# Performance work log

Hardware: AMD Instinct MI355X
Metric: run time of the kernel (lower is better)

The kernel has to match this reference:

```python
import jax, jax.numpy as jnp
import numpy as np

B, S, H = 32, 2048, 512

def setup_inputs() -> dict:
    key = jax.random.key(0)
    k1, k2, k3, k4 = jax.random.split(key, 4)
    Y = jax.random.normal(k1, (B, S, H), dtype=jnp.float32)
    mask_Y = jnp.ones((B, S), dtype=jnp.float32)
    W = jax.random.normal(k2, (H, H), dtype=jnp.float32)
    b = jax.random.normal(k3, (H,), dtype=jnp.float32)
    w = jax.random.normal(k4, (H,), dtype=jnp.float32)
    return {"Y": Y, "mask_Y": mask_Y, "W": W, "b": b, "w": w}

def reference(Y, mask_Y, W, b, w):
    # u: [B,S,H] = tanh(Y @ W + b)
    u = jnp.tanh(jnp.einsum('bsh,hd->bsd', Y, W) + b)
    # scores: [B,S] = u . w, masked with large negative additive bias
    scores = jnp.einsum('bsh,h->bs', u, w) - 1000.0 * (1.0 - mask_Y)
    alpha = jax.nn.softmax(scores, axis=1)  # [B,S]
    # c_star: [B,H] = attention-weighted sum of Y
    c_star = jnp.einsum('bs,bsh->bh', alpha, Y)
    return c_star
```

## Files before the change

### kernel.cpp

```cpp
#include <hip/hip_runtime.h>
#include <hip/hip_bf16.h>


#define Bsz 32
#define Ssz 2048
#define Hsz 512
#define Msz (Bsz * Ssz)

using half8   = __attribute__((ext_vector_type(8))) _Float16;
using floatx4 = __attribute__((ext_vector_type(4))) float;

__device__ __forceinline__ void llds16(void* l, const void* g) {
  __builtin_amdgcn_global_load_lds((const __attribute__((address_space(1))) void*)g,
                                   (__attribute__((address_space(3))) void*)l, 16, 0, 0);
}

__device__ __forceinline__ float fast_tanh(float x) {
  const float e = __expf(2.f * x);
  return 1.f - 2.f / (e + 1.f);
}

__global__ __launch_bounds__(256) void wsplit_k(const float* __restrict__ W,
                                                _Float16* __restrict__ Wt) {
  __shared__ float tile[32][33];
  const int bx = blockIdx.x & 15, by = blockIdx.x >> 4;
  const int tx = threadIdx.x & 31, ty = threadIdx.x >> 5;
#pragma unroll
  for (int i = 0; i < 4; ++i)
    tile[ty + 8 * i][tx] = W[(size_t)(by * 32 + ty + 8 * i) * Hsz + bx * 32 + tx];
  __syncthreads();
#pragma unroll
  for (int i = 0; i < 4; ++i) {
    const int n = bx * 32 + ty + 8 * i;
    const int k = by * 32 + tx;
    Wt[(size_t)n * Hsz + k] = (_Float16)tile[tx][ty + 8 * i];
  }
}

__global__ __launch_bounds__(256) void gemm_score_k(const float* __restrict__ Y,
                                                    const _Float16* __restrict__ Wt,
                                                    const float* __restrict__ bvec,
                                                    const float* __restrict__ wvec,
                                                    float* __restrict__ scores4) {
  __shared__ __align__(16) float    As[128 * 32];
  __shared__ __align__(16) _Float16 Bs[128 * 32];
  const int tid = threadIdx.x;
  const int lane = tid & 63, wv = tid >> 6;
  const int wr = wv >> 1, wc = wv & 1;
  const int lr = lane & 15, lq = lane >> 4;
  const int g = blockIdx.x;
  const int x = g & 7, q = g >> 3;
  const int nblk = q & 3;
  const int mblk = (q >> 2) * 8 + x;

  floatx4 acc[4][4];
#pragma unroll
  for (int rf = 0; rf < 4; ++rf)
#pragma unroll
    for (int cf = 0; cf < 4; ++cf)
      acc[rf][cf] = (floatx4){0.f, 0.f, 0.f, 0.f};

  const float* aY = Y + (size_t)mblk * 128 * Hsz;
  const _Float16* bW = Wt + (size_t)nblk * 128 * Hsz;

  for (int it = 0; it < 16; ++it) {
    const int k0 = it * 32;
#pragma unroll
    for (int i = 0; i < 4; ++i) {
      const int cb = i * 256 + wv * 64;
      const int p = cb + lane;
      const int row = p >> 3;
      const int gc = (p & 7) ^ (row & 7);
      llds16(&As[cb * 4], aY + (size_t)row * Hsz + k0 + gc * 4);
    }
#pragma unroll
    for (int i = 0; i < 2; ++i) {
      const int cb = i * 256 + wv * 64;
      const int p = cb + lane;
      const int row = p >> 2;
      const int gc = (p & 3) ^ ((row >> 1) & 3);
      llds16(&Bs[cb * 8], bW + (size_t)row * Hsz + k0 + gc * 8);
    }
    __syncthreads();

    half8 a[4], bf[4];
#pragma unroll
    for (int rf = 0; rf < 4; ++rf) {
      const int ar = wr * 64 + rf * 16 + lr;
      const int s0 = (lq * 2) ^ (ar & 7);
      const float4 flo = *(const float4*)&As[ar * 32 + s0 * 4];
      const float4 fhi = *(const float4*)&As[ar * 32 + (s0 ^ 1) * 4];
      half8 h;
      h[0] = (_Float16)flo.x; h[1] = (_Float16)flo.y;
      h[2] = (_Float16)flo.z; h[3] = (_Float16)flo.w;
      h[4] = (_Float16)fhi.x; h[5] = (_Float16)fhi.y;
      h[6] = (_Float16)fhi.z; h[7] = (_Float16)fhi.w;
      a[rf] = h;
    }
#pragma unroll
    for (int cf = 0; cf < 4; ++cf) {
      const int nr = wc * 64 + cf * 16 + lr;
      bf[cf] = *(const half8*)&Bs[nr * 32 + (lq ^ ((nr >> 1) & 3)) * 8];
    }
#pragma unroll
    for (int rf = 0; rf < 4; ++rf)
#pragma unroll
      for (int cf = 0; cf < 4; ++cf)
        acc[rf][cf] = __builtin_amdgcn_mfma_f32_16x16x32_f16(a[rf], bf[cf], acc[rf][cf], 0, 0, 0);
    __syncthreads();
  }

  float bb[4], ww[4];
  const int colbase = nblk * 128 + wc * 64;
#pragma unroll
  for (int cf = 0; cf < 4; ++cf) {
    const int col = colbase + cf * 16 + lr;
    bb[cf] = bvec[col];
    ww[cf] = wvec[col];
  }
  float* red = (float*)As;
#pragma unroll
  for (int rf = 0; rf < 4; ++rf) {
#pragma unroll
    for (int r = 0; r < 4; ++r) {
      float v = 0.f;
#pragma unroll
      for (int cf = 0; cf < 4; ++cf)
        v += fast_tanh(acc[rf][cf][r] + bb[cf]) * ww[cf];
      v += __shfl_xor(v, 1, 16);
      v += __shfl_xor(v, 2, 16);
      v += __shfl_xor(v, 4, 16);
      v += __shfl_xor(v, 8, 16);
      if (lr == 0)
        red[(wr * 64 + rf * 16 + lq * 4 + r) * 2 + wc] = v;
    }
  }
  __syncthreads();
  if (tid < 128)
    scores4[(size_t)nblk * Msz + mblk * 128 + tid] = red[2 * tid] + red[2 * tid + 1];
}

__global__ __launch_bounds__(256) void softmax_k(const float* __restrict__ scores4,
                                                 const float* __restrict__ mask,
                                                 float* __restrict__ alpha) {
  const int b = blockIdx.x, t = threadIdx.x;
  const int lane = t & 63, wv = t >> 6;
  float s[8];
  float mx = -3.4e38f;
#pragma unroll
  for (int i = 0; i < 8; ++i) {
    const int idx = b * Ssz + i * 256 + t;
    float v = scores4[idx] + scores4[Msz + idx] + scores4[2 * Msz + idx] + scores4[3 * Msz + idx];
    v -= 1000.f * (1.f - mask[idx]);
    s[i] = v;
    mx = fmaxf(mx, v);
  }
  for (int off = 32; off > 0; off >>= 1) mx = fmaxf(mx, __shfl_xor(mx, off, 64));
  __shared__ float rm[4], rs[4];
  if (lane == 0) rm[wv] = mx;
  __syncthreads();
  mx = fmaxf(fmaxf(rm[0], rm[1]), fmaxf(rm[2], rm[3]));
  float sum = 0.f;
#pragma unroll
  for (int i = 0; i < 8; ++i) {
    s[i] = __expf(s[i] - mx);
    sum += s[i];
  }
  for (int off = 32; off > 0; off >>= 1) sum += __shfl_xor(sum, off, 64);
  if (lane == 0) rs[wv] = sum;
  __syncthreads();
  sum = rs[0] + rs[1] + rs[2] + rs[3];
  const float inv = 1.f / sum;
#pragma unroll
  for (int i = 0; i < 8; ++i) alpha[b * Ssz + i * 256 + t] = s[i] * inv;
}

__global__ __launch_bounds__(256) void wsum1_k(const float* __restrict__ alpha,
                                               const float* __restrict__ Y,
                                               float* __restrict__ partial) {
  const int b = blockIdx.x >> 5, sc = blockIdx.x & 31;
  const int t = threadIdx.x, lane = t & 63, wv = t >> 6;
  __shared__ float part[4 * 512];
  const int s0 = sc * 64 + wv * 16;
  const float* al = alpha + b * Ssz + s0;
  const float4* Yb = (const float4*)(Y + ((size_t)b * Ssz + s0) * Hsz);
  float a0 = 0.f, a1 = 0.f, a2 = 0.f, a3 = 0.f, a4 = 0.f, a5 = 0.f, a6 = 0.f, a7 = 0.f;
#pragma unroll 4
  for (int r = 0; r < 16; ++r) {
    const float a = al[r];
    const float4 y0 = Yb[r * 128 + lane * 2];
    const float4 y1 = Yb[r * 128 + lane * 2 + 1];
    a0 = fmaf(a, y0.x, a0); a1 = fmaf(a, y0.y, a1);
    a2 = fmaf(a, y0.z, a2); a3 = fmaf(a, y0.w, a3);
    a4 = fmaf(a, y1.x, a4); a5 = fmaf(a, y1.y, a5);
    a6 = fmaf(a, y1.z, a6); a7 = fmaf(a, y1.w, a7);
  }
  part[wv * 512 + 0 * 64 + lane] = a0;
  part[wv * 512 + 1 * 64 + lane] = a1;
  part[wv * 512 + 2 * 64 + lane] = a2;
  part[wv * 512 + 3 * 64 + lane] = a3;
  part[wv * 512 + 4 * 64 + lane] = a4;
  part[wv * 512 + 5 * 64 + lane] = a5;
  part[wv * 512 + 6 * 64 + lane] = a6;
  part[wv * 512 + 7 * 64 + lane] = a7;
  __syncthreads();
#pragma unroll
  for (int i = 0; i < 2; ++i) {
    const int h = i * 256 + t;
    const int idx = (h & 7) * 64 + (h >> 3);
    partial[((size_t)(b * 32 + sc)) * Hsz + h] =
        part[idx] + part[512 + idx] + part[1024 + idx] + part[1536 + idx];
  }
}

__global__ __launch_bounds__(256) void wsum2_k(const float* __restrict__ partial,
                                               float* __restrict__ out) {
  const int b = blockIdx.x >> 1;
  const int h = (blockIdx.x & 1) * 256 + threadIdx.x;
  float s = 0.f;
#pragma unroll 8
  for (int sc = 0; sc < 32; ++sc)
    s += partial[((size_t)(b * 32 + sc)) * Hsz + h];
  out[b * Hsz + h] = s;
}

extern "C" void kernel_launch(void* const* d_in, const int* in_sizes, int n_in,
                              void* d_out, int out_size, void* d_ws, size_t ws_size,
                              hipStream_t stream) {
  (void)in_sizes; (void)n_in; (void)out_size; (void)ws_size;
  const float* Y    = (const float*)d_in[0];
  const float* mask = (const float*)d_in[1];
  const float* W    = (const float*)d_in[2];
  const float* bvec = (const float*)d_in[3];
  const float* wvec = (const float*)d_in[4];
  float* out = (float*)d_out;

  char* ws = (char*)d_ws;
  _Float16* Wt   = (_Float16*)ws;
  float* scores4 = (float*)(ws + ((size_t)1 << 20));
  float* alpha   = (float*)(ws + ((size_t)2 << 20));
  float* partial = (float*)(ws + ((size_t)3 << 20));

  wsplit_k<<<256, 256, 0, stream>>>(W, Wt);
  gemm_score_k<<<(Msz / 128) * 4, 256, 0, stream>>>(Y, Wt, bvec, wvec, scores4);
  softmax_k<<<Bsz, 256, 0, stream>>>(scores4, mask, alpha);
  wsum1_k<<<Bsz * 32, 256, 0, stream>>>(alpha, Y, partial);
  wsum2_k<<<Bsz * 2, 256, 0, stream>>>(partial, out);
}
```

Baseline: 273.4 us.

## Make GEMM persistent with full W slice resident in LDS and register-prefetched Y

```diff
diff --git a/kernel.cpp b/kernel.cpp
--- a/kernel.cpp
+++ b/kernel.cpp
@@ -37,107 +37,103 @@
   }
 }
 
-__global__ __launch_bounds__(256) void gemm_score_k(const float* __restrict__ Y,
-                                                    const _Float16* __restrict__ Wt,
-                                                    const float* __restrict__ bvec,
-                                                    const float* __restrict__ wvec,
-                                                    float* __restrict__ scores4) {
-  __shared__ __align__(16) float    As[128 * 32];
-  __shared__ __align__(16) _Float16 Bs[128 * 32];
+__global__ __launch_bounds__(256, 1) void gemm_score_k(const float* __restrict__ Y,
+                                                       const _Float16* __restrict__ Wt,
+                                                       const float* __restrict__ bvec,
+                                                       const float* __restrict__ wvec,
+                                                       float* __restrict__ scores4) {
+  __shared__ __align__(16) _Float16 Bs[128 * 512];
   const int tid = threadIdx.x;
   const int lane = tid & 63, wv = tid >> 6;
-  const int wr = wv >> 1, wc = wv & 1;
   const int lr = lane & 15, lq = lane >> 4;
   const int g = blockIdx.x;
-  const int x = g & 7, q = g >> 3;
-  const int nblk = q & 3;
-  const int mblk = (q >> 2) * 8 + x;
-
-  floatx4 acc[4][4];
-#pragma unroll
-  for (int rf = 0; rf < 4; ++rf)
-#pragma unroll
-    for (int cf = 0; cf < 4; ++cf)
-      acc[rf][cf] = (floatx4){0.f, 0.f, 0.f, 0.f};
-
-  const float* aY = Y + (size_t)mblk * 128 * Hsz;
-  const _Float16* bW = Wt + (size_t)nblk * 128 * Hsz;
-
-  for (int it = 0; it < 16; ++it) {
-    const int k0 = it * 32;
-#pragma unroll
-    for (int i = 0; i < 4; ++i) {
-      const int cb = i * 256 + wv * 64;
-      const int p = cb + lane;
-      const int row = p >> 3;
-      const int gc = (p & 7) ^ (row & 7);
-      llds16(&As[cb * 4], aY + (size_t)row * Hsz + k0 + gc * 4);
-    }
-#pragma unroll
-    for (int i = 0; i < 2; ++i) {
-      const int cb = i * 256 + wv * 64;
-      const int p = cb + lane;
-      const int row = p >> 2;
-      const int gc = (p & 3) ^ ((row >> 1) & 3);
-      llds16(&Bs[cb * 8], bW + (size_t)row * Hsz + k0 + gc * 8);
-    }
-    __syncthreads();
-
-    half8 a[4], bf[4];
-#pragma unroll
-    for (int rf = 0; rf < 4; ++rf) {
-      const int ar = wr * 64 + rf * 16 + lr;
-      const int s0 = (lq * 2) ^ (ar & 7);
-      const float4 flo = *(const float4*)&As[ar * 32 + s0 * 4];
-      const float4 fhi = *(const float4*)&As[ar * 32 + (s0 ^ 1) * 4];
-      half8 h;
-      h[0] = (_Float16)flo.x; h[1] = (_Float16)flo.y;
-      h[2] = (_Float16)flo.z; h[3] = (_Float16)flo.w;
-      h[4] = (_Float16)fhi.x; h[5] = (_Float16)fhi.y;
-      h[6] = (_Float16)fhi.z; h[7] = (_Float16)fhi.w;
-      a[rf] = h;
-    }
-#pragma unroll
-    for (int cf = 0; cf < 4; ++cf) {
-      const int nr = wc * 64 + cf * 16 + lr;
-      bf[cf] = *(const half8*)&Bs[nr * 32 + (lq ^ ((nr >> 1) & 3)) * 8];
-    }
-#pragma unroll
-    for (int rf = 0; rf < 4; ++rf)
-#pragma unroll
-      for (int cf = 0; cf < 4; ++cf)
-        acc[rf][cf] = __builtin_amdgcn_mfma_f32_16x16x32_f16(a[rf], bf[cf], acc[rf][cf], 0, 0, 0);
-    __syncthreads();
-  }
-
-  float bb[4], ww[4];
-  const int colbase = nblk * 128 + wc * 64;
-#pragma unroll
-  for (int cf = 0; cf < 4; ++cf) {
-    const int col = colbase + cf * 16 + lr;
+  const int mblk = g & 63, nblk = g >> 6;
+
+  const _Float16* Wn = Wt + (size_t)(nblk * 128) * Hsz;
+  for (int i = 0; i < 32; ++i) {
+    const int r = i * 4 + wv;
+    const int gc = lane ^ (r & 7);
+    llds16(&Bs[r * 512 + lane * 8], Wn + (size_t)r * Hsz + gc * 8);
+  }
+  float bb[8], ww[8];
+#pragma unroll
+  for (int cf = 0; cf < 8; ++cf) {
+    const int col = nblk * 128 + cf * 16 + lr;
     bb[cf] = bvec[col];
     ww[cf] = wvec[col];
   }
-  float* red = (float*)As;
-#pragma unroll
-  for (int rf = 0; rf < 4; ++rf) {
-#pragma unroll
-    for (int r = 0; r < 4; ++r) {
-      float v = 0.f;
-#pragma unroll
-      for (int cf = 0; cf < 4; ++cf)
-        v += fast_tanh(acc[rf][cf][r] + bb[cf]) * ww[cf];
-      v += __shfl_xor(v, 1, 16);
-      v += __shfl_xor(v, 2, 16);
-      v += __shfl_xor(v, 4, 16);
-      v += __shfl_xor(v, 8, 16);
-      if (lr == 0)
-        red[(wr * 64 + rf * 16 + lq * 4 + r) * 2 + wc] = v;
+  __syncthreads();
+
+  const float* aY = Y + ((size_t)(mblk * 1024 + wv * 32 + lr)) * Hsz + lq * 8;
+
+#pragma unroll 1
+  for (int mch = 0; mch < 8; ++mch) {
+    const float* am = aY + (size_t)mch * 128 * Hsz;
+    floatx4 acc[2][8];
+#pragma unroll
+    for (int rf = 0; rf < 2; ++rf)
+#pragma unroll
+      for (int cf = 0; cf < 8; ++cf)
+        acc[rf][cf] = (floatx4){0.f, 0.f, 0.f, 0.f};
+
+    float4 pa[2][2][2];
+#pragma unroll
+    for (int rf = 0; rf < 2; ++rf) {
+      const float4* p = (const float4*)(am + rf * 16 * Hsz);
+      pa[0][rf][0] = p[0];
+      pa[0][rf][1] = p[1];
     }
-  }
-  __syncthreads();
-  if (tid < 128)
-    scores4[(size_t)nblk * Msz + mblk * 128 + tid] = red[2 * tid] + red[2 * tid + 1];
+
+#pragma unroll
+    for (int it = 0; it < 16; ++it) {
+      const int cur = it & 1;
+      if (it < 15) {
+#pragma unroll
+        for (int rf = 0; rf < 2; ++rf) {
+          const float4* p = (const float4*)(am + rf * 16 * Hsz + (it + 1) * 32);
+          pa[cur ^ 1][rf][0] = p[0];
+          pa[cur ^ 1][rf][1] = p[1];
+        }
+      }
+      half8 a[2];
+#pragma unroll
+      for (int rf = 0; rf < 2; ++rf) {
+        const float4 f0 = pa[cur][rf][0], f1 = pa[cur][rf][1];
+        half8 h;
+        h[0] = (_Float16)f0.x; h[1] = (_Float16)f0.y;
+        h[2] = (_Float16)f0.z; h[3] = (_Float16)f0.w;
+        h[4] = (_Float16)f1.x; h[5] = (_Float16)f1.y;
+        h[6] = (_Float16)f1.z; h[7] = (_Float16)f1.w;
+        a[rf] = h;
+      }
+#pragma unroll
+      for (int cf = 0; cf < 8; ++cf) {
+        const int nr = cf * 16 + lr;
+        const int slot = (it * 4 + lq) ^ (nr & 7);
+        const half8 b = *(const half8*)&Bs[nr * 512 + slot * 8];
+        acc[0][cf] = __builtin_amdgcn_mfma_f32_16x16x32_f16(a[0], b, acc[0][cf], 0, 0, 0);
+        acc[1][cf] = __builtin_amdgcn_mfma_f32_16x16x32_f16(a[1], b, acc[1][cf], 0, 0, 0);
+      }
+    }
+
+#pragma unroll
+    for (int rf = 0; rf < 2; ++rf) {
+#pragma unroll
+      for (int r = 0; r < 4; ++r) {
+        float v = 0.f;
+#pragma unroll
+        for (int cf = 0; cf < 8; ++cf)
+          v += fast_tanh(acc[rf][cf][r] + bb[cf]) * ww[cf];
+        v += __shfl_xor(v, 1, 16);
+        v += __shfl_xor(v, 2, 16);
+        v += __shfl_xor(v, 4, 16);
+        v += __shfl_xor(v, 8, 16);
+        if (lr == 0)
+          scores4[(size_t)nblk * Msz + mblk * 1024 + mch * 128 + wv * 32 +
+                  rf * 16 + lq * 4 + r] = v;
+      }
+    }
+  }
 }
 
 __global__ __launch_bounds__(256) void softmax_k(const float* __restrict__ scores4,
@@ -242,7 +238,7 @@
   float* partial = (float*)(ws + ((size_t)3 << 20));
 
   wsplit_k<<<256, 256, 0, stream>>>(W, Wt);
-  gemm_score_k<<<(Msz / 128) * 4, 256, 0, stream>>>(Y, Wt, bvec, wvec, scores4);
+  gemm_score_k<<<256, 256, 0, stream>>>(Y, Wt, bvec, wvec, scores4);
   softmax_k<<<Bsz, 256, 0, stream>>>(scores4, mask, alpha);
   wsum1_k<<<Bsz * 32, 256, 0, stream>>>(alpha, Y, partial);
   wsum2_k<<<Bsz * 2, 256, 0, stream>>>(partial, out);
```

New measurement: 404.8 us. +48.1%, slower.
